# Kernel tuning notes

Hardware: AMD Instinct MI355X
Metric: run time of the kernel (lower is better)

The kernel has to match this reference:

```python
import jax, jax.numpy as jnp
import numpy as np

N = 20000
F_IN = 128
HID = 128
HEADS = 8
NCLS = 18
NEG_SLOPE = 0.2


def setup_inputs() -> dict:
    key = jax.random.key(0)
    ks = jax.random.split(key, 12)
    x = jax.random.normal(ks[0], (N, F_IN), dtype=jnp.float32)
    edge_index = jax.random.randint(ks[1], (2, 200000), 0, N)
    sc1 = 1.0 / np.sqrt(F_IN)
    sc2 = 1.0 / np.sqrt(HEADS * HID)
    W1 = jax.random.normal(ks[2], (F_IN, HEADS * HID), dtype=jnp.float32) * sc1
    a1_src = jax.random.normal(ks[3], (HEADS, HID), dtype=jnp.float32) * sc1
    a1_dst = jax.random.normal(ks[4], (HEADS, HID), dtype=jnp.float32) * sc1
    b1 = jnp.zeros((HEADS * HID,), dtype=jnp.float32)
    W2 = jax.random.normal(ks[5], (HEADS * HID, NCLS), dtype=jnp.float32) * sc2
    a2_src = jax.random.normal(ks[6], (1, NCLS), dtype=jnp.float32) * sc2
    a2_dst = jax.random.normal(ks[7], (1, NCLS), dtype=jnp.float32) * sc2
    b2 = jnp.zeros((NCLS,), dtype=jnp.float32)
    return {"x": x, "edge_index": edge_index, "W1": W1, "a1_src": a1_src,
            "a1_dst": a1_dst, "b1": b1, "W2": W2, "a2_src": a2_src,
            "a2_dst": a2_dst, "b2": b2}


def gat_conv(x, src, dst, W, a_src, a_dst, b, heads, out_ch):
    n = x.shape[0]
    h = (x @ W).reshape(n, heads, out_ch)              # [N,H,C]
    alpha_s = jnp.sum(h * a_src, axis=-1)              # [N,H]
    alpha_d = jnp.sum(h * a_dst, axis=-1)              # [N,H]
    e = jax.nn.leaky_relu(alpha_s[src] + alpha_d[dst], NEG_SLOPE)  # [E,H]
    # per-destination softmax (segment softmax)
    m = jax.ops.segment_max(e, dst, num_segments=n)
    e = jnp.exp(e - m[dst])
    z = jax.ops.segment_sum(e, dst, num_segments=n)
    alpha = e / (z[dst] + 1e-16)                       # [E,H]
    out = jax.ops.segment_sum(alpha[:, :, None] * h[src], dst, num_segments=n)
    return out.reshape(n, heads * out_ch) + b


def reference(x, edge_index, W1, a1_src, a1_dst, b1, W2, a2_src, a2_dst, b2):
    n = x.shape[0]
    # PyG GATConv adds self-loops by default
    loops = jnp.arange(n, dtype=edge_index.dtype)
    src = jnp.concatenate([edge_index[0], loops])
    dst = jnp.concatenate([edge_index[1], loops])
    h = gat_conv(x, src, dst, W1, a1_src, a1_dst, b1, HEADS, HID)
    h = jax.nn.relu(h)
    # F.dropout(training=self.training) is identity in eval mode
    out = gat_conv(h, src, dst, W2, a2_src, a2_dst, b2, 1, NCLS)
    return out
```

## Files before the change

### kernel.cpp

```cpp
#include <hip/hip_runtime.h>
#include <math.h>

#define FIN 128
#define NH 8
#define HC 128
#define HD (NH*HC)
#define NC 18
#define NCP 24
#define NEG 0.2f

typedef __attribute__((ext_vector_type(8))) short bf16x8;
typedef __attribute__((ext_vector_type(4))) float f32x4;

__device__ __forceinline__ float lrelu(float v){ return v > 0.f ? v : NEG*v; }

__device__ __forceinline__ unsigned short f2b(float f){
  unsigned u = __float_as_uint(f);
  unsigned r = (u + 0x7fffu + ((u >> 16) & 1u)) >> 16;
  return (unsigned short)r;
}
__device__ __forceinline__ float b2f_lo(unsigned u){ return __uint_as_float(u << 16); }
__device__ __forceinline__ float b2f_hi(unsigned u){ return __uint_as_float(u & 0xffff0000u); }

__device__ __forceinline__ void acc8(float* a, float w, uint4 r){
  a[0] += w*b2f_lo(r.x); a[1] += w*b2f_hi(r.x);
  a[2] += w*b2f_lo(r.y); a[3] += w*b2f_hi(r.y);
  a[4] += w*b2f_lo(r.z); a[5] += w*b2f_hi(r.z);
  a[6] += w*b2f_lo(r.w); a[7] += w*b2f_hi(r.w);
}

__global__ __launch_bounds__(1024) void scan_k(const int* __restrict__ deg, int N,
                                               int* __restrict__ off, int* __restrict__ cursor){
  __shared__ int wsum[16];
  __shared__ int s_carry;
  int t = threadIdx.x, lane = t & 63, wid = t >> 6;
  if (t == 0) s_carry = 0;
  __syncthreads();
  for (int base = 0; base < N; base += 1024) {
    int i = base + t;
    int v = (i < N) ? deg[i] : 0;
    int x = v;
    #pragma unroll
    for (int o = 1; o < 64; o <<= 1) {
      int y = __shfl_up(x, o, 64);
      if (lane >= o) x += y;
    }
    if (lane == 63) wsum[wid] = x;
    __syncthreads();
    if (wid == 0) {
      int wv = (lane < 16) ? wsum[lane] : 0;
      #pragma unroll
      for (int o = 1; o < 16; o <<= 1) {
        int y = __shfl_up(wv, o, 64);
        if (lane >= o) wv += y;
      }
      if (lane < 16) wsum[lane] = wv;
    }
    __syncthreads();
    int woff = (wid > 0) ? wsum[wid-1] : 0;
    int carry = s_carry;
    int exc = x - v + woff + carry;
    if (i < N) { off[i] = exc; cursor[i] = exc; }
    __syncthreads();
    if (t == 1023) s_carry = carry + wsum[15];
    __syncthreads();
  }
  if (t == 0) off[N] = s_carry;
}

__global__ void scatter_k(const int* __restrict__ ei, int E0, int N,
                          int* __restrict__ cursor, int* __restrict__ csr){
  int e = blockIdx.x*256 + threadIdx.x;
  int tot = E0 + N;
  if (e >= tot) return;
  int src, dst;
  if (e < E0) { src = ei[e]; dst = ei[E0 + e]; }
  else        { src = e - E0; dst = src; }
  int p = atomicAdd(&cursor[dst], 1);
  csr[p] = src;
}

__global__ __launch_bounds__(256) void prep_k(const float* __restrict__ x,
    const float* __restrict__ W1, const float* __restrict__ W2,
    const int* __restrict__ ei,
    unsigned short* __restrict__ xb, unsigned short* __restrict__ w1t,
    unsigned short* __restrict__ w2b, int* __restrict__ deg,
    int total8, int bX, int E0, int N, int bH){
  __shared__ unsigned short sT[FIN][64+2];
  int b = blockIdx.x, t = threadIdx.x;
  if (b < bX) {
    int i = b*256 + t;
    if (i < total8) {
      const float4* p = (const float4*)x + (size_t)i*2;
      float4 a = p[0], c = p[1];
      uint4 o;
      o.x = (unsigned)f2b(a.x) | ((unsigned)f2b(a.y) << 16);
      o.y = (unsigned)f2b(a.z) | ((unsigned)f2b(a.w) << 16);
      o.z = (unsigned)f2b(c.x) | ((unsigned)f2b(c.y) << 16);
      o.w = (unsigned)f2b(c.z) | ((unsigned)f2b(c.w) << 16);
      ((uint4*)xb)[i] = o;
    }
    return;
  }
  b -= bX;
  if (b < 16) {
    int n0 = b * 64;
    #pragma unroll
    for (int i = 0; i < 32; ++i) {
      int idx = i*256 + t;
      int k = idx >> 6, nl = idx & 63;
      sT[k][nl] = f2b(W1[(size_t)k*HD + n0 + nl]);
    }
    __syncthreads();
    #pragma unroll
    for (int i = 0; i < 16; ++i) {
      int nl = i*4 + (t >> 6);
      int kp = t & 63;
      unsigned u = (unsigned)sT[2*kp][nl] | ((unsigned)sT[2*kp+1][nl] << 16);
      *(unsigned*)&w1t[(size_t)(n0+nl)*FIN + 2*kp] = u;
    }
    return;
  }
  b -= 16;
  if (b < 72) {
    int idx = b*256 + t;
    if (idx < HD*NC) {
      int k = idx / NC, c = idx - k*NC;
      w2b[k*NCP + c] = f2b(W2[idx]);
    }
    return;
  }
  b -= 72;
  {
    int e = b*256 + t;
    int tot = E0 + N;
    if (e >= tot) return;
    int dst = (e < E0) ? ei[E0 + e] : (e - E0);
    atomicAdd(&deg[dst], 1);
  }
}

__global__ __launch_bounds__(256) void gemm1_mfma_k(const unsigned short* __restrict__ xb,
    const unsigned short* __restrict__ w1t,
    const float* __restrict__ a1s, const float* __restrict__ a1d,
    unsigned short* __restrict__ g1b, float* __restrict__ as1, float* __restrict__ ad1,
    int N){
  __shared__ unsigned short sA[128][136];
  __shared__ unsigned short sB[128][136];
  __shared__ float sAs[2][128], sAd[2][128];
  int t = threadIdx.x, lane = t & 63, wid = t >> 6;
  int bm = blockIdx.x * 128;
  int head = blockIdx.y;
  int bn = head * 128;
  #pragma unroll
  for (int i = 0; i < 2; ++i) {
    int idx = i*256 + t;
    int row = idx >> 2, seg = idx & 3;
    int gm = bm + row;
    uint4 a0,a1,a2,a3;
    if (gm < N) {
      const uint4* gp = (const uint4*)(xb + (size_t)gm*FIN + seg*32);
      a0 = gp[0]; a1 = gp[1]; a2 = gp[2]; a3 = gp[3];
    } else {
      a0 = a1 = a2 = a3 = make_uint4(0,0,0,0);
    }
    uint4* lp = (uint4*)&sA[row][seg*32];
    lp[0]=a0; lp[1]=a1; lp[2]=a2; lp[3]=a3;
  }
  #pragma unroll
  for (int i = 0; i < 2; ++i) {
    int idx = i*256 + t;
    int row = idx >> 2, seg = idx & 3;
    const uint4* gp = (const uint4*)(w1t + (size_t)(bn + row)*FIN + seg*32);
    uint4* lp = (uint4*)&sB[row][seg*32];
    lp[0]=gp[0]; lp[1]=gp[1]; lp[2]=gp[2]; lp[3]=gp[3];
  }
  __syncthreads();
  int wr = wid >> 1, wc = wid & 1;
  int lr = lane & 15, kb = lane >> 4;
  f32x4 acc[4][4];
  #pragma unroll
  for (int mi = 0; mi < 4; ++mi)
    #pragma unroll
    for (int ni = 0; ni < 4; ++ni) {
      f32x4 z = {0.f, 0.f, 0.f, 0.f};
      acc[mi][ni] = z;
    }
  #pragma unroll
  for (int ks = 0; ks < 4; ++ks) {
    int ko = ks*32 + kb*8;
    bf16x8 a[4], b[4];
    #pragma unroll
    for (int mi = 0; mi < 4; ++mi)
      a[mi] = *(const bf16x8*)&sA[wr*64 + mi*16 + lr][ko];
    #pragma unroll
    for (int ni = 0; ni < 4; ++ni)
      b[ni] = *(const bf16x8*)&sB[wc*64 + ni*16 + lr][ko];
    #pragma unroll
    for (int mi = 0; mi < 4; ++mi)
      #pragma unroll
      for (int ni = 0; ni < 4; ++ni)
        acc[mi][ni] = __builtin_amdgcn_mfma_f32_16x16x32_bf16(a[mi], b[ni], acc[mi][ni], 0, 0, 0);
  }
  __syncthreads();

  float a1sv[4], a1dv[4];
  #pragma unroll
  for (int ni = 0; ni < 4; ++ni) {
    int c = wc*64 + ni*16 + lr;
    a1sv[ni] = a1s[head*HC + c];
    a1dv[ni] = a1d[head*HC + c];
  }
  #pragma unroll
  for (int mi = 0; mi < 4; ++mi) {
    #pragma unroll
    for (int r = 0; r < 4; ++r) {
      float ps = acc[mi][0][r]*a1sv[0] + acc[mi][1][r]*a1sv[1]
               + acc[mi][2][r]*a1sv[2] + acc[mi][3][r]*a1sv[3];
      float pd = acc[mi][0][r]*a1dv[0] + acc[mi][1][r]*a1dv[1]
               + acc[mi][2][r]*a1dv[2] + acc[mi][3][r]*a1dv[3];
      #pragma unroll
      for (int o = 1; o < 16; o <<= 1) {
        ps += __shfl_xor(ps, o, 64);
        pd += __shfl_xor(pd, o, 64);
      }
      if (lr == 0) {
        int row = wr*64 + mi*16 + kb*4 + r;
        sAs[wc][row] = ps;
        sAd[wc][row] = pd;
      }
    }
  }
  #pragma unroll
  for (int mi = 0; mi < 4; ++mi)
    #pragma unroll
    for (int ni = 0; ni < 4; ++ni) {
      int col = wc*64 + ni*16 + lr;
      #pragma unroll
      for (int r = 0; r < 4; ++r)
        sA[wr*64 + mi*16 + kb*4 + r][col] = f2b(acc[mi][ni][r]);
    }
  __syncthreads();
  {
    int row = t >> 1, half = t & 1;
    int grow = bm + row;
    if (grow < N) {
      uint4* dst = (uint4*)(g1b + (size_t)grow*HD + bn + half*64);
      const uint4* src = (const uint4*)&sA[row][half*64];
      #pragma unroll
      for (int q = 0; q < 8; ++q) dst[q] = src[q];
    }
    if (t < 128 && bm + t < N) {
      as1[(size_t)(bm + t)*NH + head] = sAs[0][t] + sAs[1][t];
      ad1[(size_t)(bm + t)*NH + head] = sAd[0][t] + sAd[1][t];
    }
  }
}

__global__ __launch_bounds__(256) void attn1_k(const unsigned short* __restrict__ g1b,
    const float* __restrict__ as1, const float* __restrict__ ad1,
    const int* __restrict__ off, const int* __restrict__ csr,
    const float* __restrict__ b1, unsigned short* __restrict__ hb, int N){
  int t = threadIdx.x, lane = t & 63, wid = t >> 6;
  int d = blockIdx.x*4 + wid;
  if (d >= N) return;
  int beg = off[d], deg = off[d+1] - beg;
  int hg = lane >> 3;
  float adg = ad1[d*NH + hg];
  float m = -1e30f, z = 0.f;
  float acc[16];
  #pragma unroll
  for (int i = 0; i < 16; ++i) acc[i] = 0.f;

  int j = 0;
  for (; j + 4 <= deg; j += 4) {
    int s0 = csr[beg+j+0], s1 = csr[beg+j+1], s2 = csr[beg+j+2], s3 = csr[beg+j+3];
    const uint4* p0 = (const uint4*)(g1b + (size_t)s0*HD) + lane*2;
    const uint4* p1 = (const uint4*)(g1b + (size_t)s1*HD) + lane*2;
    const uint4* p2 = (const uint4*)(g1b + (size_t)s2*HD) + lane*2;
    const uint4* p3 = (const uint4*)(g1b + (size_t)s3*HD) + lane*2;
    uint4 r00 = p0[0], r01 = p0[1];
    uint4 r10 = p1[0], r11 = p1[1];
    uint4 r20 = p2[0], r21 = p2[1];
    uint4 r30 = p3[0], r31 = p3[1];
    float e0 = lrelu(as1[s0*NH+hg] + adg);
    float e1 = lrelu(as1[s1*NH+hg] + adg);
    float e2 = lrelu(as1[s2*NH+hg] + adg);
    float e3 = lrelu(as1[s3*NH+hg] + adg);
    float em = fmaxf(fmaxf(e0,e1), fmaxf(e2,e3));
    if (em > m) {
      float sc = __expf(m - em);
      z *= sc;
      #pragma unroll
      for (int i = 0; i < 16; ++i) acc[i] *= sc;
      m = em;
    }
    float w0 = __expf(e0 - m), w1 = __expf(e1 - m);
    float w2 = __expf(e2 - m), w3 = __expf(e3 - m);
    z += w0 + w1 + w2 + w3;
    acc8(acc, w0, r00); acc8(acc+8, w0, r01);
    acc8(acc, w1, r10); acc8(acc+8, w1, r11);
    acc8(acc, w2, r20); acc8(acc+8, w2, r21);
    acc8(acc, w3, r30); acc8(acc+8, w3, r31);
  }
  for (; j < deg; ++j) {
    int s = csr[beg+j];
    const uint4* p = (const uint4*)(g1b + (size_t)s*HD) + lane*2;
    uint4 r0 = p[0], r1 = p[1];
    float e = lrelu(as1[s*NH+hg] + adg);
    if (e > m) {
      float sc = __expf(m - e);
      z *= sc;
      #pragma unroll
      for (int i = 0; i < 16; ++i) acc[i] *= sc;
      m = e;
    }
    float w = __expf(e - m);
    z += w;
    acc8(acc, w, r0); acc8(acc+8, w, r1);
  }

  float zinv = 1.f / (z + 1e-16f);
  int cb = lane*16;
  uint o[8];
  #pragma unroll
  for (int q = 0; q < 4; ++q) {
    float4 bv = *(const float4*)&b1[cb + q*4];
    float v0 = fmaxf(acc[q*4+0]*zinv + bv.x, 0.f);
    float v1 = fmaxf(acc[q*4+1]*zinv + bv.y, 0.f);
    float v2 = fmaxf(acc[q*4+2]*zinv + bv.z, 0.f);
    float v3 = fmaxf(acc[q*4+3]*zinv + bv.w, 0.f);
    o[q*2+0] = (unsigned)f2b(v0) | ((unsigned)f2b(v1) << 16);
    o[q*2+1] = (unsigned)f2b(v2) | ((unsigned)f2b(v3) << 16);
  }
  uint4* dst = (uint4*)(hb + (size_t)d*HD) + lane*2;
  dst[0] = make_uint4(o[0], o[1], o[2], o[3]);
  dst[1] = make_uint4(o[4], o[5], o[6], o[7]);
}

__global__ __launch_bounds__(256) void gemm2_k(const unsigned short* __restrict__ hb,
    const unsigned short* __restrict__ w2b, const float* __restrict__ a2s_g, const float* __restrict__ a2d_g,
    float* __restrict__ g2, float* __restrict__ as2, float* __restrict__ ad2, int N){
  __shared__ float red[3][64][NC+1];
  int t = threadIdx.x, lane = t & 63, wid = t >> 6;
  int n0 = blockIdx.x * 64;
  int n = n0 + lane;
  bool valid = (n < N);
  float acc[NC];
  #pragma unroll
  for (int c = 0; c < NC; ++c) acc[c] = 0.f;
  int k0beg = wid * 256;
  for (int k0 = k0beg; k0 < k0beg + 256; k0 += 8) {
    uint4 raw = valid ? *(const uint4*)(hb + (size_t)n*HD + k0) : make_uint4(0,0,0,0);
    float a[8];
    a[0]=b2f_lo(raw.x); a[1]=b2f_hi(raw.x); a[2]=b2f_lo(raw.y); a[3]=b2f_hi(raw.y);
    a[4]=b2f_lo(raw.z); a[5]=b2f_hi(raw.z); a[6]=b2f_lo(raw.w); a[7]=b2f_hi(raw.w);
    #pragma unroll
    for (int kk = 0; kk < 8; ++kk) {
      const unsigned* wr = (const unsigned*)(w2b + (size_t)(k0 + kk)*NCP);
      uint4 u0 = *(const uint4*)(wr);
      uint4 u1 = *(const uint4*)(wr + 4);
      unsigned u2 = wr[8];
      float av = a[kk];
      acc[0]  += av * b2f_lo(u0.x); acc[1]  += av * b2f_hi(u0.x);
      acc[2]  += av * b2f_lo(u0.y); acc[3]  += av * b2f_hi(u0.y);
      acc[4]  += av * b2f_lo(u0.z); acc[5]  += av * b2f_hi(u0.z);
      acc[6]  += av * b2f_lo(u0.w); acc[7]  += av * b2f_hi(u0.w);
      acc[8]  += av * b2f_lo(u1.x); acc[9]  += av * b2f_hi(u1.x);
      acc[10] += av * b2f_lo(u1.y); acc[11] += av * b2f_hi(u1.y);
      acc[12] += av * b2f_lo(u1.z); acc[13] += av * b2f_hi(u1.z);
      acc[14] += av * b2f_lo(u1.w); acc[15] += av * b2f_hi(u1.w);
      acc[16] += av * b2f_lo(u2);   acc[17] += av * b2f_hi(u2);
    }
  }
  if (wid > 0) {
    #pragma unroll
    for (int c = 0; c < NC; ++c) red[wid-1][lane][c] = acc[c];
  }
  __syncthreads();
  if (wid == 0 && valid) {
    float tot[NC];
    #pragma unroll
    for (int c = 0; c < NC; ++c)
      tot[c] = acc[c] + red[0][lane][c] + red[1][lane][c] + red[2][lane][c];
    float s = 0.f, dd = 0.f;
    #pragma unroll
    for (int c = 0; c < NC; ++c) {
      s  += tot[c]*a2s_g[c];
      dd += tot[c]*a2d_g[c];
      g2[(size_t)n*NC + c] = tot[c];
    }
    as2[n] = s; ad2[n] = dd;
  }
}

__global__ __launch_bounds__(256) void attn2_k(const float* __restrict__ g2,
    const float* __restrict__ as2, const float* __restrict__ ad2,
    const int* __restrict__ off, const int* __restrict__ csr,
    const float* __restrict__ b2, float* __restrict__ out, int N){
  int t = threadIdx.x, lane = t & 63, wid = t >> 6;
  int d = blockIdx.x*4 + wid;
  if (d >= N) return;
  int beg = off[d], deg = off[d+1] - beg;
  float adv = ad2[d];
  int g = lane / 18;
  int c = lane - g*18;
  float m = -1e30f, z = 0.f, acc = 0.f;
  if (g < 3) {
    int j = g;
    for (; j + 3 < deg; j += 6) {
      int sa = csr[beg+j], sb = csr[beg+j+3];
      float va = g2[(size_t)sa*NC + c];
      float vb = g2[(size_t)sb*NC + c];
      float ea = lrelu(as2[sa] + adv);
      float eb = lrelu(as2[sb] + adv);
      float em = fmaxf(ea, eb);
      if (em > m) { float sc = __expf(m - em); z *= sc; acc *= sc; m = em; }
      float wa = __expf(ea - m), wb = __expf(eb - m);
      z += wa + wb;
      acc += wa*va + wb*vb;
    }
    for (; j < deg; j += 3) {
      int s = csr[beg+j];
      float v = g2[(size_t)s*NC + c];
      float e = lrelu(as2[s] + adv);
      if (e > m) { float sc = __expf(m - e); z *= sc; acc *= sc; m = e; }
      float w = __expf(e - m);
      z += w;
      acc += w*v;
    }
  }
  float m0 = __shfl(m, 0),  m1 = __shfl(m, 18), m2 = __shfl(m, 36);
  float M  = fmaxf(m0, fmaxf(m1, m2));
  float e0 = __expf(m0 - M), e1 = __expf(m1 - M), e2 = __expf(m2 - M);
  float z0 = __shfl(z, 0),  z1 = __shfl(z, 18), z2 = __shfl(z, 36);
  int cl = (lane < NC) ? lane : 0;
  float a0 = __shfl(acc, cl), a1 = __shfl(acc, cl+18), a2 = __shfl(acc, cl+36);
  if (lane < NC) {
    float Z = z0*e0 + z1*e1 + z2*e2;
    float A = a0*e0 + a1*e1 + a2*e2;
    out[(size_t)d*NC + lane] = A / (Z + 1e-16f) + b2[lane];
  }
}

extern "C" void kernel_launch(void* const* d_in, const int* in_sizes, int n_in,
                              void* d_out, int out_size, void* d_ws, size_t ws_size,
                              hipStream_t stream){
  const float* x   = (const float*)d_in[0];
  const int*   ei  = (const int*)d_in[1];
  const float* W1  = (const float*)d_in[2];
  const float* a1s = (const float*)d_in[3];
  const float* a1d = (const float*)d_in[4];
  const float* b1  = (const float*)d_in[5];
  const float* W2  = (const float*)d_in[6];
  const float* a2s = (const float*)d_in[7];
  const float* a2d = (const float*)d_in[8];
  const float* b2  = (const float*)d_in[9];
  float* out = (float*)d_out;
  int N  = in_sizes[0] / FIN;
  int E0 = in_sizes[1] / 2;
  int Etot = E0 + N;

  float* as1 = (float*)d_ws;
  float* ad1 = as1 + (size_t)N*NH;
  float* g2  = ad1 + (size_t)N*NH;
  float* as2 = g2 + (size_t)N*NC;
  float* ad2 = as2 + N;
  unsigned short* g1b = (unsigned short*)(ad2 + N);
  unsigned short* hb  = g1b + (size_t)N*HD;
  int* deg    = (int*)(hb + (size_t)N*HD);
  int* off    = deg + N;
  int* cursor = off + N + 4;
  int* csr    = cursor + N;
  unsigned short* w2b = (unsigned short*)(csr + Etot);
  unsigned short* xb  = hb;
  unsigned short* w1t = hb + (size_t)N*FIN;

  hipMemsetAsync(deg, 0, sizeof(int)*(size_t)N, stream);

  int total8 = N*FIN/8;
  int bX = (total8 + 255)/256;
  int bH = (Etot + 255)/256;
  prep_k<<<bX + 16 + 72 + bH, 256, 0, stream>>>(x, W1, W2, ei, xb, w1t, w2b, deg,
                                                total8, bX, E0, N, bH);
  scan_k<<<1, 1024, 0, stream>>>(deg, N, off, cursor);
  scatter_k<<<(Etot+255)/256, 256, 0, stream>>>(ei, E0, N, cursor, csr);

  dim3 g1grid((N+127)/128, HD/128);
  gemm1_mfma_k<<<g1grid, 256, 0, stream>>>(xb, w1t, a1s, a1d, g1b, as1, ad1, N);
  attn1_k<<<(N+3)/4, 256, 0, stream>>>(g1b, as1, ad1, off, csr, b1, hb, N);
  gemm2_k<<<(N+63)/64, 256, 0, stream>>>(hb, w2b, a2s, a2d, g2, as2, ad2, N);
  attn2_k<<<(N+3)/4, 256, 0, stream>>>(g2, as2, ad2, off, csr, b2, out, N);
}
```

Measured before the change: 293.2 us.

## Use bf16 MFMA for layer-2 GEMM and serialize-per-thread prefix scan

The second-layer projection (N x 1024 by 1024 x 18) moves from scalar FMA over bf16-unpacked values to 16x16x32 bf16 MFMA instructions. W2 is pre-transposed and zero-padded to 32 output columns, and each of four waves reduces a K quarter, with partial sums combined through shared memory. The single-block degree scan changes from a loop of 1024-wide block scans with many barriers to a per-thread chunk sum, one block scan and a sequential write-out. The costs are wasted MFMA work on the padding columns and strided, less coalesced memory access in the scan.

```diff
diff --git a/kernel.cpp b/kernel.cpp
--- a/kernel.cpp
+++ b/kernel.cpp
@@ -6,7 +6,7 @@
 #define HC 128
 #define HD (NH*HC)
 #define NC 18
-#define NCP 24
+#define NW2 32
 #define NEG 0.2f
 
 typedef __attribute__((ext_vector_type(8))) short bf16x8;
@@ -32,40 +32,42 @@
 __global__ __launch_bounds__(1024) void scan_k(const int* __restrict__ deg, int N,
                                                int* __restrict__ off, int* __restrict__ cursor){
   __shared__ int wsum[16];
-  __shared__ int s_carry;
   int t = threadIdx.x, lane = t & 63, wid = t >> 6;
-  if (t == 0) s_carry = 0;
+  int PER = (N + 1023) >> 10;
+  int base = t * PER;
+  int sum = 0;
+  for (int i = 0; i < PER; ++i) {
+    int idx = base + i;
+    if (idx < N) sum += deg[idx];
+  }
+  int x = sum;
+  #pragma unroll
+  for (int o = 1; o < 64; o <<= 1) {
+    int y = __shfl_up(x, o, 64);
+    if (lane >= o) x += y;
+  }
+  if (lane == 63) wsum[wid] = x;
   __syncthreads();
-  for (int base = 0; base < N; base += 1024) {
-    int i = base + t;
-    int v = (i < N) ? deg[i] : 0;
-    int x = v;
-    #pragma unroll
-    for (int o = 1; o < 64; o <<= 1) {
-      int y = __shfl_up(x, o, 64);
-      if (lane >= o) x += y;
-    }
-    if (lane == 63) wsum[wid] = x;
-    __syncthreads();
-    if (wid == 0) {
-      int wv = (lane < 16) ? wsum[lane] : 0;
-      #pragma unroll
-      for (int o = 1; o < 16; o <<= 1) {
-        int y = __shfl_up(wv, o, 64);
-        if (lane >= o) wv += y;
-      }
-      if (lane < 16) wsum[lane] = wv;
-    }
-    __syncthreads();
-    int woff = (wid > 0) ? wsum[wid-1] : 0;
-    int carry = s_carry;
-    int exc = x - v + woff + carry;
-    if (i < N) { off[i] = exc; cursor[i] = exc; }
-    __syncthreads();
-    if (t == 1023) s_carry = carry + wsum[15];
-    __syncthreads();
-  }
-  if (t == 0) off[N] = s_carry;
+  if (wid == 0 && lane < 16) {
+    int wv = wsum[lane];
+    #pragma unroll
+    for (int o = 1; o < 16; o <<= 1) {
+      int y = __shfl_up(wv, o, 16);
+      if (lane >= o) wv += y;
+    }
+    wsum[lane] = wv;
+  }
+  __syncthreads();
+  int carry = x - sum + (wid > 0 ? wsum[wid-1] : 0);
+  int run = carry;
+  for (int i = 0; i < PER; ++i) {
+    int idx = base + i;
+    if (idx < N) {
+      off[idx] = run; cursor[idx] = run;
+      run += deg[idx];
+    }
+  }
+  if (base < N && base + PER >= N) off[N] = run;
 }
 
 __global__ void scatter_k(const int* __restrict__ ei, int E0, int N,
@@ -84,8 +86,8 @@
     const float* __restrict__ W1, const float* __restrict__ W2,
     const int* __restrict__ ei,
     unsigned short* __restrict__ xb, unsigned short* __restrict__ w1t,
-    unsigned short* __restrict__ w2b, int* __restrict__ deg,
-    int total8, int bX, int E0, int N, int bH){
+    unsigned short* __restrict__ w2t, int* __restrict__ deg,
+    int total8, int bX, int E0, int N){
   __shared__ unsigned short sT[FIN][64+2];
   int b = blockIdx.x, t = threadIdx.x;
   if (b < bX) {
@@ -122,15 +124,13 @@
     return;
   }
   b -= 16;
-  if (b < 72) {
+  if (b < (NW2*HD)/256) {
     int idx = b*256 + t;
-    if (idx < HD*NC) {
-      int k = idx / NC, c = idx - k*NC;
-      w2b[k*NCP + c] = f2b(W2[idx]);
-    }
+    int n = idx >> 10, k = idx & 1023;
+    w2t[idx] = (n < NC) ? f2b(W2[(size_t)k*NC + n]) : (unsigned short)0;
     return;
   }
-  b -= 72;
+  b -= (NW2*HD)/256;
   {
     int e = b*256 + t;
     int tot = E0 + N;
@@ -339,58 +339,73 @@
 }
 
 __global__ __launch_bounds__(256) void gemm2_k(const unsigned short* __restrict__ hb,
-    const unsigned short* __restrict__ w2b, const float* __restrict__ a2s_g, const float* __restrict__ a2d_g,
+    const unsigned short* __restrict__ w2t, const float* __restrict__ a2s_g, const float* __restrict__ a2d_g,
     float* __restrict__ g2, float* __restrict__ as2, float* __restrict__ ad2, int N){
-  __shared__ float red[3][64][NC+1];
+  __shared__ float red[4][32][32];
   int t = threadIdx.x, lane = t & 63, wid = t >> 6;
-  int n0 = blockIdx.x * 64;
-  int n = n0 + lane;
-  bool valid = (n < N);
-  float acc[NC];
-  #pragma unroll
-  for (int c = 0; c < NC; ++c) acc[c] = 0.f;
-  int k0beg = wid * 256;
-  for (int k0 = k0beg; k0 < k0beg + 256; k0 += 8) {
-    uint4 raw = valid ? *(const uint4*)(hb + (size_t)n*HD + k0) : make_uint4(0,0,0,0);
-    float a[8];
-    a[0]=b2f_lo(raw.x); a[1]=b2f_hi(raw.x); a[2]=b2f_lo(raw.y); a[3]=b2f_hi(raw.y);
-    a[4]=b2f_lo(raw.z); a[5]=b2f_hi(raw.z); a[6]=b2f_lo(raw.w); a[7]=b2f_hi(raw.w);
-    #pragma unroll
-    for (int kk = 0; kk < 8; ++kk) {
-      const unsigned* wr = (const unsigned*)(w2b + (size_t)(k0 + kk)*NCP);
-      uint4 u0 = *(const uint4*)(wr);
-      uint4 u1 = *(const uint4*)(wr + 4);
-      unsigned u2 = wr[8];
-      float av = a[kk];
-      acc[0]  += av * b2f_lo(u0.x); acc[1]  += av * b2f_hi(u0.x);
-      acc[2]  += av * b2f_lo(u0.y); acc[3]  += av * b2f_hi(u0.y);
-      acc[4]  += av * b2f_lo(u0.z); acc[5]  += av * b2f_hi(u0.z);
-      acc[6]  += av * b2f_lo(u0.w); acc[7]  += av * b2f_hi(u0.w);
-      acc[8]  += av * b2f_lo(u1.x); acc[9]  += av * b2f_hi(u1.x);
-      acc[10] += av * b2f_lo(u1.y); acc[11] += av * b2f_hi(u1.y);
-      acc[12] += av * b2f_lo(u1.z); acc[13] += av * b2f_hi(u1.z);
-      acc[14] += av * b2f_lo(u1.w); acc[15] += av * b2f_hi(u1.w);
-      acc[16] += av * b2f_lo(u2);   acc[17] += av * b2f_hi(u2);
-    }
-  }
-  if (wid > 0) {
-    #pragma unroll
-    for (int c = 0; c < NC; ++c) red[wid-1][lane][c] = acc[c];
-  }
+  int bm = blockIdx.x * 32;
+  int lr = lane & 15, kb = lane >> 4;
+  int kw = wid * 256;
+  f32x4 acc[2][2];
+  #pragma unroll
+  for (int mi = 0; mi < 2; ++mi)
+    #pragma unroll
+    for (int ni = 0; ni < 2; ++ni) {
+      f32x4 z = {0.f,0.f,0.f,0.f};
+      acc[mi][ni] = z;
+    }
+  bf16x8 zf;
+  #pragma unroll
+  for (int q = 0; q < 8; ++q) zf[q] = 0;
+  int r0n = bm + lr, r1n = bm + 16 + lr;
+  #pragma unroll
+  for (int ks = 0; ks < 8; ++ks) {
+    int k = kw + ks*32 + kb*8;
+    bf16x8 a0 = (r0n < N) ? *(const bf16x8*)&hb[(size_t)r0n*HD + k] : zf;
+    bf16x8 a1 = (r1n < N) ? *(const bf16x8*)&hb[(size_t)r1n*HD + k] : zf;
+    bf16x8 b0 = *(const bf16x8*)&w2t[(size_t)lr*HD + k];
+    bf16x8 b1 = *(const bf16x8*)&w2t[(size_t)(16+lr)*HD + k];
+    acc[0][0] = __builtin_amdgcn_mfma_f32_16x16x32_bf16(a0, b0, acc[0][0], 0,0,0);
+    acc[0][1] = __builtin_amdgcn_mfma_f32_16x16x32_bf16(a0, b1, acc[0][1], 0,0,0);
+    acc[1][0] = __builtin_amdgcn_mfma_f32_16x16x32_bf16(a1, b0, acc[1][0], 0,0,0);
+    acc[1][1] = __builtin_amdgcn_mfma_f32_16x16x32_bf16(a1, b1, acc[1][1], 0,0,0);
+  }
+  #pragma unroll
+  for (int mi = 0; mi < 2; ++mi)
+    #pragma unroll
+    for (int ni = 0; ni < 2; ++ni)
+      #pragma unroll
+      for (int r = 0; r < 4; ++r)
+        red[wid][mi*16 + kb*4 + r][ni*16 + lr] = acc[mi][ni][r];
   __syncthreads();
-  if (wid == 0 && valid) {
-    float tot[NC];
-    #pragma unroll
-    for (int c = 0; c < NC; ++c)
-      tot[c] = acc[c] + red[0][lane][c] + red[1][lane][c] + red[2][lane][c];
-    float s = 0.f, dd = 0.f;
-    #pragma unroll
-    for (int c = 0; c < NC; ++c) {
-      s  += tot[c]*a2s_g[c];
-      dd += tot[c]*a2d_g[c];
-      g2[(size_t)n*NC + c] = tot[c];
-    }
-    as2[n] = s; ad2[n] = dd;
+  int row = t >> 3;
+  int c4 = (t & 7) * 4;
+  float tot[4];
+  #pragma unroll
+  for (int q = 0; q < 4; ++q)
+    tot[q] = red[0][row][c4+q] + red[1][row][c4+q] + red[2][row][c4+q] + red[3][row][c4+q];
+  int n = bm + row;
+  float ps = 0.f, pd = 0.f;
+  #pragma unroll
+  for (int q = 0; q < 4; ++q) {
+    int c = c4 + q;
+    if (c < NC) {
+      ps += tot[q]*a2s_g[c];
+      pd += tot[q]*a2d_g[c];
+    }
+  }
+  #pragma unroll
+  for (int o = 1; o < 8; o <<= 1) {
+    ps += __shfl_xor(ps, o, 8);
+    pd += __shfl_xor(pd, o, 8);
+  }
+  if (n < N) {
+    #pragma unroll
+    for (int q = 0; q < 4; ++q) {
+      int c = c4 + q;
+      if (c < NC) g2[(size_t)n*NC + c] = tot[q];
+    }
+    if ((t & 7) == 0) { as2[n] = ps; ad2[n] = pd; }
   }
 }
 
@@ -472,7 +487,7 @@
   int* off    = deg + N;
   int* cursor = off + N + 4;
   int* csr    = cursor + N;
-  unsigned short* w2b = (unsigned short*)(csr + Etot);
+  unsigned short* w2t = (unsigned short*)(csr + Etot);
   unsigned short* xb  = hb;
   unsigned short* w1t = hb + (size_t)N*FIN;
 
@@ -481,14 +496,15 @@
   int total8 = N*FIN/8;
   int bX = (total8 + 255)/256;
   int bH = (Etot + 255)/256;
-  prep_k<<<bX + 16 + 72 + bH, 256, 0, stream>>>(x, W1, W2, ei, xb, w1t, w2b, deg,
-                                                total8, bX, E0, N, bH);
+  int bW2 = (NW2*HD)/256;
+  prep_k<<<bX + 16 + bW2 + bH, 256, 0, stream>>>(x, W1, W2, ei, xb, w1t, w2t, deg,
+                                                 total8, bX, E0, N);
   scan_k<<<1, 1024, 0, stream>>>(deg, N, off, cursor);
   scatter_k<<<(Etot+255)/256, 256, 0, stream>>>(ei, E0, N, cursor, csr);
 
   dim3 g1grid((N+127)/128, HD/128);
   gemm1_mfma_k<<<g1grid, 256, 0, stream>>>(xb, w1t, a1s, a1d, g1b, as1, ad1, N);
   attn1_k<<<(N+3)/4, 256, 0, stream>>>(g1b, as1, ad1, off, csr, b1, hb, N);
-  gemm2_k<<<(N+63)/64, 256, 0, stream>>>(hb, w2b, a2s, a2d, g2, as2, ad2, N);
+  gemm2_k<<<(N+31)/32, 256, 0, stream>>>(hb, w2t, a2s, a2d, g2, as2, ad2, N);
   attn2_k<<<(N+3)/4, 256, 0, stream>>>(g2, as2, ad2, off, csr, b2, out, N);
 }
```

New measurement: 265.4 us. 1.1x faster.
